# Optimization experiments

Hardware: AMD Instinct MI355X
Metric: run time of the kernel (lower is better)

The kernel has to match this reference:

```python
import jax, jax.numpy as jnp
from jax import lax
import numpy as np

B, N, C = 4, 2048, 64          # batch, num points, feature channels
M = 512                         # num centroids (FPS)
SAMPLES = (32, 64)              # neighbors per scale
RADII = (0.2, 0.4)              # ball radii per scale
MLPS = ((67, 64, 64, 128), (67, 128, 128, 256))  # in->hidden->out per scale (in = C + 3)


def setup_inputs() -> dict:
    key = jax.random.key(0)
    ks = jax.random.split(key, 16)
    inp = {
        "points": jax.random.uniform(ks[0], (B, 3, N), jnp.float32),   # unit cube
        "features": jax.random.normal(ks[1], (B, C, N), jnp.float32),
    }
    k = 2
    for s, dims in enumerate(MLPS):
        for l in range(3):
            cin, cout = dims[l], dims[l + 1]
            inp[f"w{s}_{l}"] = (jax.random.normal(ks[k], (cout, cin), jnp.float32)
                                * jnp.float32(1.0 / np.sqrt(cin)))
            inp[f"b{s}_{l}"] = jnp.zeros((cout,), jnp.float32)
            k += 1
    return inp


def fps(xyz, m):
    """Farthest point sampling. xyz: (B,N,3) -> indices (B,m) int32."""
    b, n, _ = xyz.shape
    big = jnp.asarray(1e10, xyz.dtype)

    def step(carry, _):
        dist, cur = carry                                   # (B,N), (B,)
        cur_pt = jnp.take_along_axis(xyz, cur[:, None, None], axis=1)  # (B,1,3)
        d2 = jnp.sum((xyz - cur_pt) ** 2, axis=-1)          # (B,N)
        dist = jnp.minimum(dist, d2)
        nxt = jnp.argmax(dist, axis=-1).astype(jnp.int32)
        return (dist, nxt), cur

    init = (jnp.full((b, n), big, xyz.dtype), jnp.zeros((b,), jnp.int32))
    _, idxs = lax.scan(step, init, None, length=m)          # (m,B)
    return idxs.T                                           # (B,m)


def ball_group(xyz, feat_t, cent, s, r):
    """Ball query + group gather. Returns (B,M,s,3+C) = [rel_xyz; features]."""
    n = xyz.shape[1]
    d2 = jnp.sum((cent[:, :, None, :] - xyz[:, None, :, :]) ** 2, axis=-1)  # (B,M,N)
    keys = jnp.where(d2 <= r * r, jnp.arange(n, dtype=jnp.int32), n)
    idx = jnp.sort(keys, axis=-1)[:, :, :s]                 # first s in-ball indices
    idx = jnp.where(idx < n, idx, idx[:, :, :1])            # pad with first valid
    gxyz = jax.vmap(lambda p, i: p[i])(xyz, idx) - cent[:, :, None, :]  # (B,M,s,3)
    gfeat = jax.vmap(lambda f, i: f[i])(feat_t, idx)        # (B,M,s,C)
    return jnp.concatenate([gxyz, gfeat], axis=-1)


def mlp_max(g, ws, bs):
    """Shared 1x1-conv MLP over (B,M,S,Cin), max over neighbor dim S."""
    x = g
    for w, b in zip(ws, bs):
        x = jax.nn.relu(jnp.einsum('bmsc,oc->bmso', x, w) + b)
    return jnp.max(x, axis=2)                               # (B,M,Cout)


def reference(points, features,
              w0_0, b0_0, w0_1, b0_1, w0_2, b0_2,
              w1_0, b1_0, w1_1, b1_1, w1_2, b1_2):
    xyz = jnp.transpose(points, (0, 2, 1))                  # (B,N,3)
    feat_t = jnp.transpose(features, (0, 2, 1))             # (B,N,C)
    idx = fps(xyz, M)                                       # (B,M)
    cent = jnp.take_along_axis(xyz, idx[:, :, None], axis=1)  # (B,M,3)
    Ws = [(w0_0, w0_1, w0_2), (w1_0, w1_1, w1_2)]
    Bs = [(b0_0, b0_1, b0_2), (b1_0, b1_1, b1_2)]
    outs = []
    for i, (s, r) in enumerate(zip(SAMPLES, RADII)):
        g = ball_group(xyz, feat_t, cent, s, r)             # (B,M,s,3+C)
        outs.append(mlp_max(g, Ws[i], Bs[i]))               # (B,M,Cout_i)
    feat = jnp.transpose(jnp.concatenate(outs, axis=-1), (0, 2, 1))  # (B,384,M)
    return jnp.transpose(cent, (0, 2, 1)), feat             # (B,3,M), (B,384,M)
```

## Files before the change

kernel.cpp:

```cpp
#include <hip/hip_runtime.h>

#define NPTS 2048
#define BATCH 4
#define CFEAT 64
#define MCENT 512

typedef float f4 __attribute__((ext_vector_type(4)));
typedef float f2 __attribute__((ext_vector_type(2)));
typedef short s8v __attribute__((ext_vector_type(8)));

__device__ __forceinline__ unsigned short f2bf(float x) {
    unsigned u = __float_as_uint(x);
    return (unsigned short)((u + 0x7fffu + ((u >> 16) & 1u)) >> 16);
}

template <int CTRL>
__device__ __forceinline__ float dpp_max_step(float v) {
    int t = __builtin_amdgcn_update_dpp(0, __float_as_int(v), CTRL, 0xf, 0xf, true);
    return fmaxf(v, __int_as_float(t));
}

template <int COUT, int CIN, int KPW, bool PERM>
__device__ void pack_seg(const float* w, unsigned short* dst, int start, int stride) {
    for (int i = start; i < COUT * KPW; i += stride) {
        int o = i / KPW, k = i - o * KPW;
        float v = 0.f;
        if (PERM) {
            if (k < 64) v = w[o * CIN + 3 + k];
            else if (k < 67) v = w[o * CIN + (k - 64)];
        } else {
            if (k < CIN) v = w[o * CIN + k];
        }
        dst[i] = f2bf(v);
    }
}

__global__ __launch_bounds__(256, 1) void fps_prep(
    const float* __restrict__ pts, const float* __restrict__ feats,
    const float* w00, const float* w01, const float* w02,
    const float* w10, const float* w11, const float* w12,
    float* cent, unsigned short* ftr, unsigned short* wp, float* out)
{
    const int tid = threadIdx.x;
    if (blockIdx.x >= 4) {
        const int stride = 64 * 256;
        const int start = (blockIdx.x - 4) * 256 + tid;
        for (int i = start; i < BATCH * NPTS * CFEAT; i += stride) {
            int c = i & 63, n = (i >> 6) & (NPTS - 1), b = i >> 17;
            ftr[i] = f2bf(feats[(b * CFEAT + c) * NPTS + n]);
        }
        pack_seg<64, 67, 96, true>(w00, wp + 0, start, stride);
        pack_seg<64, 64, 64, false>(w01, wp + 6144, start, stride);
        pack_seg<128, 64, 64, false>(w02, wp + 10240, start, stride);
        pack_seg<128, 67, 96, true>(w10, wp + 18432, start, stride);
        pack_seg<128, 128, 128, false>(w11, wp + 30720, start, stride);
        pack_seg<256, 128, 128, false>(w12, wp + 47104, start, stride);
        return;
    }
    const int b = blockIdx.x;
    const int lane = tid & 63, wv = tid >> 6;
    const float* px = pts + b * 3 * NPTS;
    const float* py = px + NPTS;
    const float* pz = py + NPTS;
    __shared__ __align__(16) float4 slotq[8 * 2];
    __shared__ __align__(16) float4 scent[MCENT];

    const int base = wv * 512 + lane * 8;
    f2 rx[4], ry[4], rz[4], rd[4];
#pragma unroll
    for (int i = 0; i < 4; ++i) {
        rx[i] = *(const f2*)(px + base + 2 * i);
        ry[i] = *(const f2*)(py + base + 2 * i);
        rz[i] = *(const f2*)(pz + base + 2 * i);
        rd[i] = (f2){1e10f, 1e10f};
    }
    float cx = px[0], cy = py[0], cz = pz[0];
    int par = 0;
    for (int m = 0; m < MCENT; ++m) {
        if (tid == 0) scent[m] = make_float4(cx, cy, cz, 0.f);
        {
#pragma clang fp contract(off)
            f2 c2x = {cx, cx}, c2y = {cy, cy}, c2z = {cz, cz};
#pragma unroll
            for (int i = 0; i < 4; ++i) {
                f2 dx = rx[i] - c2x, dy = ry[i] - c2y, dz = rz[i] - c2z;
                f2 d2 = dx * dx + dy * dy;
                d2 = d2 + dz * dz;
                f2 old = rd[i];
                f2 nd;
                nd.x = fminf(old.x, d2.x);
                nd.y = fminf(old.y, d2.y);
                rd[i] = nd;
            }
        }
        float n0 = rd[0].x, n1 = rd[0].y, n2 = rd[1].x, n3 = rd[1].y;
        float n4 = rd[2].x, n5 = rd[2].y, n6 = rd[3].x, n7 = rd[3].y;
        float bv = fmaxf(fmaxf(fmaxf(n0, n1), fmaxf(n2, n3)),
                         fmaxf(fmaxf(n4, n5), fmaxf(n6, n7)));
        float ox = rx[3].y, oy = ry[3].y, oz = rz[3].y;
        {
            float ndv[8] = {n0, n1, n2, n3, n4, n5, n6, n7};
#pragma unroll
            for (int k = 6; k >= 0; --k) {
                bool t = (ndv[k] == bv);
                float nx = (k & 1) ? rx[k >> 1].y : rx[k >> 1].x;
                float ny = (k & 1) ? ry[k >> 1].y : ry[k >> 1].x;
                float nz = (k & 1) ? rz[k >> 1].y : rz[k >> 1].x;
                ox = t ? nx : ox; oy = t ? ny : oy; oz = t ? nz : oz;
            }
        }
        float v = bv;
        v = dpp_max_step<0x111>(v);
        v = dpp_max_step<0x112>(v);
        v = dpp_max_step<0x114>(v);
        v = dpp_max_step<0x118>(v);
        v = dpp_max_step<0x142>(v);
        v = dpp_max_step<0x143>(v);
        float wmax = __int_as_float(__builtin_amdgcn_readlane(__float_as_int(v), 63));
        unsigned long long cand = __ballot(bv == wmax);
        int wl = __ffsll(cand) - 1;
        if (lane == wl) slotq[(par * 4 + wv) * 2] = make_float4(bv, ox, oy, oz);
        __syncthreads();
        float4 s0 = slotq[(par * 4 + 0) * 2];
        float4 s1 = slotq[(par * 4 + 1) * 2];
        float4 s2 = slotq[(par * 4 + 2) * 2];
        float4 s3 = slotq[(par * 4 + 3) * 2];
        float4 c01 = (s1.x > s0.x) ? s1 : s0;
        float4 c23 = (s3.x > s2.x) ? s3 : s2;
        float4 cc  = (c23.x > c01.x) ? c23 : c01;
        cx = cc.y; cy = cc.z; cz = cc.w;
        par ^= 1;
    }
    __syncthreads();
    float* outc = out + b * 3 * MCENT;
    for (int m = tid; m < MCENT; m += 256) {
        float4 c = scent[m];
        float* cw = cent + (b * MCENT + m) * 3;
        cw[0] = c.x; cw[1] = c.y; cw[2] = c.z;
        outc[m] = c.x; outc[MCENT + m] = c.y; outc[2 * MCENT + m] = c.z;
    }
}

template <int MT, int KSTEPS, int NTW>
__device__ __forceinline__ void layer_mm(const unsigned short* A, const unsigned short* __restrict__ Wg,
                                         const float* __restrict__ bias, int lane, int wv,
                                         f4 (&acc)[MT][NTW])
{
    constexpr int KP = KSTEPS * 32;
    const int r15 = lane & 15, g = lane >> 4;
#pragma unroll
    for (int nt = 0; nt < NTW; ++nt) {
        int n = (wv * NTW + nt) * 16 + r15;
        float bv = bias[n];
#pragma unroll
        for (int mt = 0; mt < MT; ++mt) acc[mt][nt] = (f4){bv, bv, bv, bv};
    }
#pragma unroll
    for (int ks = 0; ks < KSTEPS; ++ks) {
        s8v afr[MT];
#pragma unroll
        for (int mt = 0; mt < MT; ++mt) {
            int row = mt * 16 + r15;
            int byte = ((row * KP + ks * 32 + g * 8) * 2) ^ ((row & 7) << 4);
            afr[mt] = *(const s8v*)((const char*)A + byte);
        }
#pragma unroll
        for (int nt = 0; nt < NTW; ++nt) {
            int n = (wv * NTW + nt) * 16 + r15;
            s8v bfr = *(const s8v*)(Wg + n * KP + ks * 32 + g * 8);
#pragma unroll
            for (int mt = 0; mt < MT; ++mt)
                acc[mt][nt] = __builtin_amdgcn_mfma_f32_16x16x32_bf16(afr[mt], bfr, acc[mt][nt], 0, 0, 0);
        }
    }
}

template <int MT, int NTW, int CO>
__device__ __forceinline__ void store_lds(f4 (&acc)[MT][NTW], unsigned short* OUT, int lane, int wv) {
    const int r15 = lane & 15, g = lane >> 4;
#pragma unroll
    for (int mt = 0; mt < MT; ++mt)
#pragma unroll
        for (int nt = 0; nt < NTW; ++nt)
#pragma unroll
            for (int q = 0; q < 4; ++q) {
                int j = mt * 16 + g * 4 + q;
                int n = (wv * NTW + nt) * 16 + r15;
                float v = fmaxf(acc[mt][nt][q], 0.f);
                int byte = ((j * CO + n) * 2) ^ ((j & 7) << 4);
                *(unsigned short*)((char*)OUT + byte) = f2bf(v);
            }
}

template <int S_, int C1, int C2, int C3>
__device__ __forceinline__ void msg_body(int bm, char* smem,
    const float* __restrict__ pts, const unsigned short* __restrict__ ftr,
    const float* __restrict__ cent,
    const unsigned short* __restrict__ W0, const float* __restrict__ B0,
    const unsigned short* __restrict__ W1, const float* __restrict__ B1,
    const unsigned short* __restrict__ W2, const float* __restrict__ B2,
    float* __restrict__ outf, int ch_off, float rr)
{
    constexpr int MT = S_ / 16;
    constexpr int KS1 = C1 / 32, KS2 = C2 / 32;
    constexpr int NW1 = C1 / 64, NW2 = C2 / 64, NW3 = C3 / 64;
    constexpr int HA = (S_ * 96 > S_ * C2) ? S_ * 96 : S_ * C2;
    unsigned short* hA = (unsigned short*)smem;
    unsigned short* hB = hA + HA;
    int* nbr = (int*)(hB + S_ * C1);
    int* wtot = nbr + S_;
    const int tid = threadIdx.x, lane = tid & 63, wv = tid >> 6;
    const int b = bm >> 9, m = bm & (MCENT - 1);
    const float cx = cent[bm * 3], cy = cent[bm * 3 + 1], cz = cent[bm * 3 + 2];
    const float* px = pts + b * 3 * NPTS;
    const float* py = px + NPTS;
    const float* pz = py + NPTS;

    unsigned mask = 0; int cnt = 0;
    {
#pragma clang fp contract(off)
#pragma unroll
        for (int k = 0; k < 8; ++k) {
            int n = tid * 8 + k;
            float dx = cx - px[n], dy = cy - py[n], dz = cz - pz[n];
            float d2 = dx * dx + dy * dy;
            d2 = d2 + dz * dz;
            if (d2 <= rr) { mask |= 1u << k; ++cnt; }
        }
    }
    int inc = cnt;
#pragma unroll
    for (int off = 1; off < 64; off <<= 1) {
        int t = __shfl_up(inc, off);
        if (lane >= off) inc += t;
    }
    if (lane == 63) wtot[wv] = inc;
    __syncthreads();
    int base = 0, tot = 0;
#pragma unroll
    for (int w = 0; w < 4; ++w) { int t = wtot[w]; tot += t; if (w < wv) base += t; }
    int pos = base + inc - cnt;
#pragma unroll
    for (int k = 0; k < 8; ++k) {
        if ((mask >> k) & 1) {
            if (pos < S_) nbr[pos] = tid * 8 + k;
            ++pos;
        }
    }
    __syncthreads();
    const int first = nbr[0];

    for (int e = tid; e < S_ * 8; e += 256) {
        int j = e >> 3, c8 = e & 7;
        int p = (j < tot) ? nbr[j] : first;
        s8v v = *(const s8v*)(ftr + (b * NPTS + p) * 64 + c8 * 8);
        int byte = ((j * 96 + c8 * 8) * 2) ^ ((j & 7) << 4);
        *(s8v*)((char*)hA + byte) = v;
    }
    for (int e = tid; e < S_ * 4; e += 256) {
        int j = e >> 2, q = e & 3;
        int p = (j < tot) ? nbr[j] : first;
        s8v v = {0, 0, 0, 0, 0, 0, 0, 0};
        if (q == 0) {
            v[0] = (short)f2bf(px[p] - cx);
            v[1] = (short)f2bf(py[p] - cy);
            v[2] = (short)f2bf(pz[p] - cz);
        }
        int byte = ((j * 96 + 64 + q * 8) * 2) ^ ((j & 7) << 4);
        *(s8v*)((char*)hA + byte) = v;
    }
    __syncthreads();

    {
        f4 acc[MT][NW1];
        layer_mm<MT, 3, NW1>(hA, W0, B0, lane, wv, acc);
        store_lds<MT, NW1, C1>(acc, hB, lane, wv);
    }
    __syncthreads();
    {
        f4 acc[MT][NW2];
        layer_mm<MT, KS1, NW2>(hB, W1, B1, lane, wv, acc);
        store_lds<MT, NW2, C2>(acc, hA, lane, wv);
    }
    __syncthreads();
    {
        f4 acc[MT][NW3];
        layer_mm<MT, KS2, NW3>(hA, W2, B2, lane, wv, acc);
        const int r15 = lane & 15;
        float* dst = outf + b * 384 * MCENT + ch_off * MCENT + m;
#pragma unroll
        for (int nt = 0; nt < NW3; ++nt) {
            float mv = -1e30f;
#pragma unroll
            for (int mt = 0; mt < MT; ++mt)
#pragma unroll
                for (int q = 0; q < 4; ++q) mv = fmaxf(mv, acc[mt][nt][q]);
            mv = fmaxf(mv, __shfl_xor(mv, 16));
            mv = fmaxf(mv, __shfl_xor(mv, 32));
            float v = fmaxf(mv, 0.f);
            if (lane < 16) dst[((wv * NW3 + nt) * 16 + r15) * MCENT] = v;
        }
    }
}

__global__ __launch_bounds__(256) void msg_both(
    const float* __restrict__ pts, const unsigned short* __restrict__ ftr,
    const float* __restrict__ cent, const unsigned short* __restrict__ wp,
    const float* __restrict__ b00, const float* __restrict__ b01, const float* __restrict__ b02,
    const float* __restrict__ b10, const float* __restrict__ b11, const float* __restrict__ b12,
    float* __restrict__ outf, float rr0, float rr1)
{
    extern __shared__ __align__(16) char smem[];
    if (blockIdx.x < BATCH * MCENT)
        msg_body<32, 64, 64, 128>(blockIdx.x, smem, pts, ftr, cent,
                                  wp + 0, b00, wp + 6144, b01, wp + 10240, b02, outf, 0, rr0);
    else
        msg_body<64, 128, 128, 256>(blockIdx.x - BATCH * MCENT, smem, pts, ftr, cent,
                                    wp + 18432, b10, wp + 30720, b11, wp + 47104, b12, outf, 128, rr1);
}

extern "C" void kernel_launch(void* const* d_in, const int* in_sizes, int n_in,
                              void* d_out, int out_size, void* d_ws, size_t ws_size,
                              hipStream_t stream) {
    const float* pts  = (const float*)d_in[0];
    const float* feats = (const float*)d_in[1];
    const float* w00 = (const float*)d_in[2];  const float* b00 = (const float*)d_in[3];
    const float* w01 = (const float*)d_in[4];  const float* b01 = (const float*)d_in[5];
    const float* w02 = (const float*)d_in[6];  const float* b02 = (const float*)d_in[7];
    const float* w10 = (const float*)d_in[8];  const float* b10 = (const float*)d_in[9];
    const float* w11 = (const float*)d_in[10]; const float* b11 = (const float*)d_in[11];
    const float* w12 = (const float*)d_in[12]; const float* b12 = (const float*)d_in[13];
    float* out = (float*)d_out;
    char* ws = (char*)d_ws;
    float* cent = (float*)ws;
    unsigned short* ftr = (unsigned short*)(ws + 24576);
    unsigned short* wp  = (unsigned short*)(ws + 24576 + 1048576);

    hipLaunchKernelGGL(fps_prep, dim3(68), dim3(256), 0, stream,
                       pts, feats, w00, w01, w02, w10, w11, w12, cent, ftr, wp, out);
    float* outf = out + BATCH * 3 * MCENT;
    const float RR0 = (float)(0.2 * 0.2);
    const float RR1 = (float)(0.4 * 0.4);
    hipLaunchKernelGGL(msg_both, dim3(2 * BATCH * MCENT), dim3(256), 33040, stream,
                       pts, ftr, cent, wp, b00, b01, b02, b10, b11, b12, outf, RR0, RR1);
}
```

Before: 302.9 us.

## Spread FPS over 1024 threads with 2 points per lane and DPP cross-wave reduction

```diff
diff --git a/kernel.cpp b/kernel.cpp
--- a/kernel.cpp
+++ b/kernel.cpp
@@ -18,6 +18,10 @@
 __device__ __forceinline__ float dpp_max_step(float v) {
     int t = __builtin_amdgcn_update_dpp(0, __float_as_int(v), CTRL, 0xf, 0xf, true);
     return fmaxf(v, __int_as_float(t));
+}
+
+__device__ __forceinline__ float readlane_f(float v, int l) {
+    return __int_as_float(__builtin_amdgcn_readlane(__float_as_int(v), l));
 }
 
 template <int COUT, int CIN, int KPW, bool PERM>
@@ -35,7 +39,7 @@
     }
 }
 
-__global__ __launch_bounds__(256, 1) void fps_prep(
+__global__ __launch_bounds__(1024, 1) void fps_prep(
     const float* __restrict__ pts, const float* __restrict__ feats,
     const float* w00, const float* w01, const float* w02,
     const float* w10, const float* w11, const float* w12,
@@ -43,8 +47,8 @@
 {
     const int tid = threadIdx.x;
     if (blockIdx.x >= 4) {
-        const int stride = 64 * 256;
-        const int start = (blockIdx.x - 4) * 256 + tid;
+        const int stride = 16 * 1024;
+        const int start = (blockIdx.x - 4) * 1024 + tid;
         for (int i = start; i < BATCH * NPTS * CFEAT; i += stride) {
             int c = i & 63, n = (i >> 6) & (NPTS - 1), b = i >> 17;
             ftr[i] = f2bf(feats[(b * CFEAT + c) * NPTS + n]);
@@ -62,53 +66,34 @@
     const float* px = pts + b * 3 * NPTS;
     const float* py = px + NPTS;
     const float* pz = py + NPTS;
-    __shared__ __align__(16) float4 slotq[8 * 2];
     __shared__ __align__(16) float4 scent[MCENT];
-
-    const int base = wv * 512 + lane * 8;
-    f2 rx[4], ry[4], rz[4], rd[4];
-#pragma unroll
-    for (int i = 0; i < 4; ++i) {
-        rx[i] = *(const f2*)(px + base + 2 * i);
-        ry[i] = *(const f2*)(py + base + 2 * i);
-        rz[i] = *(const f2*)(pz + base + 2 * i);
-        rd[i] = (f2){1e10f, 1e10f};
-    }
+    __shared__ __align__(16) float4 slotq[2][16];
+
+    const int base = wv * 128 + lane * 2;
+    f2 rx = *(const f2*)(px + base);
+    f2 ry = *(const f2*)(py + base);
+    f2 rz = *(const f2*)(pz + base);
+    f2 rd = (f2){1e10f, 1e10f};
     float cx = px[0], cy = py[0], cz = pz[0];
     int par = 0;
     for (int m = 0; m < MCENT; ++m) {
         if (tid == 0) scent[m] = make_float4(cx, cy, cz, 0.f);
+        f2 nd;
         {
 #pragma clang fp contract(off)
             f2 c2x = {cx, cx}, c2y = {cy, cy}, c2z = {cz, cz};
-#pragma unroll
-            for (int i = 0; i < 4; ++i) {
-                f2 dx = rx[i] - c2x, dy = ry[i] - c2y, dz = rz[i] - c2z;
-                f2 d2 = dx * dx + dy * dy;
-                d2 = d2 + dz * dz;
-                f2 old = rd[i];
-                f2 nd;
-                nd.x = fminf(old.x, d2.x);
-                nd.y = fminf(old.y, d2.y);
-                rd[i] = nd;
-            }
-        }
-        float n0 = rd[0].x, n1 = rd[0].y, n2 = rd[1].x, n3 = rd[1].y;
-        float n4 = rd[2].x, n5 = rd[2].y, n6 = rd[3].x, n7 = rd[3].y;
-        float bv = fmaxf(fmaxf(fmaxf(n0, n1), fmaxf(n2, n3)),
-                         fmaxf(fmaxf(n4, n5), fmaxf(n6, n7)));
-        float ox = rx[3].y, oy = ry[3].y, oz = rz[3].y;
-        {
-            float ndv[8] = {n0, n1, n2, n3, n4, n5, n6, n7};
-#pragma unroll
-            for (int k = 6; k >= 0; --k) {
-                bool t = (ndv[k] == bv);
-                float nx = (k & 1) ? rx[k >> 1].y : rx[k >> 1].x;
-                float ny = (k & 1) ? ry[k >> 1].y : ry[k >> 1].x;
-                float nz = (k & 1) ? rz[k >> 1].y : rz[k >> 1].x;
-                ox = t ? nx : ox; oy = t ? ny : oy; oz = t ? nz : oz;
-            }
-        }
+            f2 dx = rx - c2x, dy = ry - c2y, dz = rz - c2z;
+            f2 d2 = dx * dx + dy * dy;
+            d2 = d2 + dz * dz;
+            nd.x = fminf(rd.x, d2.x);
+            nd.y = fminf(rd.y, d2.y);
+            rd = nd;
+        }
+        bool oddW = nd.y > nd.x;
+        float bv = oddW ? nd.y : nd.x;
+        float ox = oddW ? rx.y : rx.x;
+        float oy = oddW ? ry.y : ry.x;
+        float oz = oddW ? rz.y : rz.x;
         float v = bv;
         v = dpp_max_step<0x111>(v);
         v = dpp_max_step<0x112>(v);
@@ -116,24 +101,29 @@
         v = dpp_max_step<0x118>(v);
         v = dpp_max_step<0x142>(v);
         v = dpp_max_step<0x143>(v);
-        float wmax = __int_as_float(__builtin_amdgcn_readlane(__float_as_int(v), 63));
-        unsigned long long cand = __ballot(bv == wmax);
+        float wmaxw = readlane_f(v, 63);
+        unsigned long long cand = __ballot(bv == wmaxw);
         int wl = __ffsll(cand) - 1;
-        if (lane == wl) slotq[(par * 4 + wv) * 2] = make_float4(bv, ox, oy, oz);
+        if (lane == wl) slotq[par][wv] = make_float4(bv, ox, oy, oz);
         __syncthreads();
-        float4 s0 = slotq[(par * 4 + 0) * 2];
-        float4 s1 = slotq[(par * 4 + 1) * 2];
-        float4 s2 = slotq[(par * 4 + 2) * 2];
-        float4 s3 = slotq[(par * 4 + 3) * 2];
-        float4 c01 = (s1.x > s0.x) ? s1 : s0;
-        float4 c23 = (s3.x > s2.x) ? s3 : s2;
-        float4 cc  = (c23.x > c01.x) ? c23 : c01;
-        cx = cc.y; cy = cc.z; cz = cc.w;
+        float4 sv4 = slotq[par][lane & 15];
+        float sv = sv4.x;
+        float r = sv;
+        r = dpp_max_step<0x111>(r);
+        r = dpp_max_step<0x112>(r);
+        r = dpp_max_step<0x114>(r);
+        r = dpp_max_step<0x118>(r);
+        float wmax = readlane_f(r, 15);
+        unsigned long long c2 = __ballot(sv == wmax) & 0xFFFFull;
+        int ws = __ffsll(c2) - 1;
+        cx = readlane_f(sv4.y, ws);
+        cy = readlane_f(sv4.z, ws);
+        cz = readlane_f(sv4.w, ws);
         par ^= 1;
     }
     __syncthreads();
     float* outc = out + b * 3 * MCENT;
-    for (int m = tid; m < MCENT; m += 256) {
+    for (int m = tid; m < MCENT; m += 1024) {
         float4 c = scent[m];
         float* cw = cent + (b * MCENT + m) * 3;
         cw[0] = c.x; cw[1] = c.y; cw[2] = c.z;
@@ -336,7 +326,7 @@
     unsigned short* ftr = (unsigned short*)(ws + 24576);
     unsigned short* wp  = (unsigned short*)(ws + 24576 + 1048576);
 
-    hipLaunchKernelGGL(fps_prep, dim3(68), dim3(256), 0, stream,
+    hipLaunchKernelGGL(fps_prep, dim3(20), dim3(1024), 0, stream,
                        pts, feats, w00, w01, w02, w10, w11, w12, cent, ftr, wp, out);
     float* outf = out + BATCH * 3 * MCENT;
     const float RR0 = (float)(0.2 * 0.2);
```

Result: slower. 357.3 us (+18.0%).
